# Kernel optimization log

Hardware: AMD Instinct MI355X
Metric: run time of the kernel (lower is better)

The kernel has to match this reference:

```python
import jax, jax.numpy as jnp
import numpy as np

B, S, H, OUT, L = 32, 4096, 128, 128, 3


def _log_g(x):
    return jnp.where(x >= 0, jnp.log(jax.nn.relu(x) + 0.5), -jax.nn.softplus(-x))


def _cell(x, Wz, bz, Wh, bh):
    # x: [B, S, Din] -> h: [B, S, H]
    k = x @ Wz.T + bz                              # [B,S,H]
    log_z = -jax.nn.softplus(-k)
    log_coeffs = -jax.nn.softplus(k)
    # h_0 = zeros -> log_g(0) = log(0.5)
    log_h0 = jnp.full((x.shape[0], 1, k.shape[-1]), np.log(0.5), dtype=k.dtype)
    log_tilde_h = _log_g(x @ Wh.T + bh)
    log_values = jnp.concatenate([log_h0, log_z + log_tilde_h], axis=1)  # [B,S+1,H]
    # FAITHFUL to source: cumsum over the FEATURE axis (dim=-1), pad along seq
    a_star = jnp.pad(jnp.cumsum(log_coeffs, axis=-1), ((0, 0), (1, 0), (0, 0)))
    log_h = a_star + jax.lax.cumlogsumexp(log_values - a_star, axis=1)
    # torch forward applies sigmoid to the cell output, then drops the h_0 row
    return jax.nn.sigmoid(jnp.exp(log_h))[:, 1:, :]


def setup_inputs() -> dict:
    key = jax.random.key(0)
    ks = jax.random.split(key, 2 * L + 2)
    inp = {"x": jax.random.normal(ks[0], (B, S), dtype=jnp.float32)}
    for l in range(L):
        din = 1 if l == 0 else H
        inp[f"Wz{l}"] = jax.random.normal(ks[1 + 2 * l], (H, din), dtype=jnp.float32) * 0.02
        inp[f"bz{l}"] = jnp.zeros((H,), dtype=jnp.float32)
        inp[f"Wh{l}"] = jax.random.normal(ks[2 + 2 * l], (H, din), dtype=jnp.float32) * 0.02
        inp[f"bh{l}"] = jnp.zeros((H,), dtype=jnp.float32)
    inp["Wout"] = jax.random.normal(ks[-1], (OUT, H * S), dtype=jnp.float32) * (1.0 / np.sqrt(H * S))
    inp["bout"] = jnp.zeros((OUT,), dtype=jnp.float32)
    return inp


def reference(x, Wz0, bz0, Wh0, bh0, Wz1, bz1, Wh1, bh1, Wz2, bz2, Wh2, bh2, Wout, bout):
    h = x[:, :, None]  # [B,S,1]
    for (Wz, bz, Wh, bh) in ((Wz0, bz0, Wh0, bh0), (Wz1, bz1, Wh1, bh1), (Wz2, bz2, Wh2, bh2)):
        h = _cell(h, Wz, bz, Wh, bh)
    flat = h.reshape(h.shape[0], -1)  # [B, S*H]
    return flat @ Wout.T + bout       # [B, OUT]
```

## Files before the change

### kernel.cpp

```cpp
#include <hip/hip_runtime.h>
#include <hip/hip_bf16.h>
#include <math.h>

#define B_   32
#define S_   4096
#define H_   128
#define OUT_ 128
#define P_   (B_*S_)
#define NC_  64
#define CH_  (S_/NC_)
#define NKS_ 512
#define KTOT_ (H_*S_)
#define NEGINF_ (-__builtin_inff())
#define HTP_ 136

typedef __bf16 bf16x8 __attribute__((ext_vector_type(8)));
typedef float  f32x4  __attribute__((ext_vector_type(4)));
typedef unsigned short ushort8_t __attribute__((ext_vector_type(8)));

__device__ __forceinline__ float sp_(float x) {
  return __logf(1.f + __expf(x));
}
__device__ __forceinline__ float logg_(float x) {
  float t = (x >= 0.f) ? (x + 0.5f) : __builtin_amdgcn_rcpf(1.f + __expf(-x));
  return __logf(t);
}
__device__ __forceinline__ float lae_(float a, float b) {
  float m = fmaxf(a, b);
  float d = -fabsf(a - b);
  return m + __logf(1.f + __expf(d));
}
__device__ __forceinline__ float sigm_(float e) {
  return __builtin_amdgcn_rcpf(1.f + __expf(-e));
}
__device__ __forceinline__ unsigned short f2bf_(float f) {
  unsigned int u = __float_as_uint(f);
  u += 0x7fffu + ((u >> 16) & 1u);
  return (unsigned short)(u >> 16);
}

#define DPPADD_(v, ctrl, rmask) \
  ((v) + __int_as_float(__builtin_amdgcn_update_dpp( \
      0, __float_as_int(v), (ctrl), (rmask), 0xf, true)))
__device__ __forceinline__ float wscan_(float v) {
  v = DPPADD_(v, 0x111, 0xf);
  v = DPPADD_(v, 0x112, 0xf);
  v = DPPADD_(v, 0x114, 0xf);
  v = DPPADD_(v, 0x118, 0xf);
  v = DPPADD_(v, 0x142, 0xa);
  v = DPPADD_(v, 0x143, 0xc);
  return v;
}

__global__ __launch_bounds__(256) void convw2_kernel(
    const float* __restrict__ Wz1, const float* __restrict__ Wh1,
    const float* __restrict__ Wz2, const float* __restrict__ Wh2,
    unsigned short* __restrict__ Wc1, unsigned short* __restrict__ Wc2)
{
  int idx = blockIdx.x * 256 + threadIdx.x;
  Wc1[idx] = f2bf_(idx < 16384 ? Wz1[idx] : Wh1[idx - 16384]);
  Wc2[idx] = f2bf_(idx < 16384 ? Wz2[idx] : Wh2[idx - 16384]);
}

__global__ __launch_bounds__(256) void prep0t_kernel(
    const float* __restrict__ x,
    const float* __restrict__ Wz, const float* __restrict__ bz,
    const float* __restrict__ Wh, const float* __restrict__ bh,
    float* __restrict__ u, float* __restrict__ A, float* __restrict__ tot)
{
  __shared__ float tpart[4][128];
  int lane = threadIdx.x & 63, w = threadIdx.x >> 6;
  float wz0 = Wz[lane], wz1 = Wz[lane + 64];
  float bz0 = bz[lane], bz1 = bz[lane + 64];
  float wh0 = Wh[lane], wh1 = Wh[lane + 64];
  float bh0 = bh[lane], bh1 = bh[lane + 64];
  int blk = blockIdx.x;
  size_t base = (size_t)blk * (CH_ * H_);
  int pos0 = blk * CH_;
  float t0 = NEGINF_, t1 = NEGINF_;
  for (int j = 0; j < 16; ++j) {
    int i = j * 4 + w;
    float xv = x[pos0 + i];
    float k0 = fmaf(xv, wz0, bz0), k1 = fmaf(xv, wz1, bz1);
    float g0 = fmaf(xv, wh0, bh0), g1 = fmaf(xv, wh1, bh1);
    float lc0 = -sp_(k0), lc1 = -sp_(k1);
    float lv0 = k0 + lc0 + logg_(g0);
    float lv1 = k1 + lc1 + logg_(g1);
    float s0 = wscan_(lc0);
    float c0 = __shfl(s0, 63, 64);
    float s1 = wscan_(lc1) + c0;
    float u0 = lv0 - s0, u1 = lv1 - s1;
    size_t o = base + (size_t)i * H_;
    u[o + lane]      = u0;  u[o + 64 + lane] = u1;
    A[o + lane]      = s0;  A[o + 64 + lane] = s1;
    t0 = lae_(t0, u0); t1 = lae_(t1, u1);
  }
  tpart[w][lane] = t0; tpart[w][64 + lane] = t1;
  __syncthreads();
  if (w == 0) {
    int ch = lane;
    tot[(size_t)blk * H_ + ch] =
        lae_(lae_(tpart[0][ch], tpart[1][ch]), lae_(tpart[2][ch], tpart[3][ch]));
    ch = lane + 64;
    tot[(size_t)blk * H_ + ch] =
        lae_(lae_(tpart[0][ch], tpart[1][ch]), lae_(tpart[2][ch], tpart[3][ch]));
  }
}

__global__ __launch_bounds__(128) void scan2_kernel(
    const float* __restrict__ tot, float* __restrict__ carry)
{
  int b = blockIdx.x, ch = threadIdx.x;
  float r = -0.6931471805599453f;
  for (int c = 0; c < NC_; ++c) {
    size_t idx = (size_t)(b * NC_ + c) * H_ + ch;
    carry[idx] = r;
    r = lae_(r, tot[idx]);
  }
}

__global__ __launch_bounds__(256) void kb_kernel(
    const float* __restrict__ carry,
    const unsigned short* __restrict__ Wc,
    const float* __restrict__ bz, const float* __restrict__ bh,
    float* __restrict__ u, float* __restrict__ A,
    float* __restrict__ tot)
{
  __shared__ unsigned short hT[64][HTP_];
  __shared__ float kg[16][260];
  __shared__ float scr[32][128];
  __shared__ float thand[128];
  __shared__ float tpart[4][128];
  int tid = threadIdx.x;
  int lane = tid & 63, w = tid >> 6;
  int l15 = lane & 15, quad = lane >> 4;
  int half = tid >> 7, ch = tid & 127;
  int blk = blockIdx.x;
  size_t base = (size_t)blk * (CH_ * H_);

  if (half == 0) {
    float r = carry[(size_t)blk * H_ + ch];
    const float* up = u + base + ch;
    const float* Ap = A + base + ch;
    for (int i0 = 0; i0 < 32; i0 += 16) {
      float uv[16], av[16];
      #pragma unroll
      for (int i = 0; i < 16; ++i) { uv[i] = up[(i0 + i) * H_]; av[i] = Ap[(i0 + i) * H_]; }
      #pragma unroll
      for (int i = 0; i < 16; ++i) {
        r = lae_(r, uv[i]);
        hT[i0 + i][ch] = f2bf_(sigm_(__expf(av[i] + r)));
      }
    }
    thand[ch] = r;
  } else {
    float r = NEGINF_;
    const float* up = u + base + ch;
    for (int i0 = 0; i0 < 32; i0 += 16) {
      float uv[16];
      #pragma unroll
      for (int i = 0; i < 16; ++i) uv[i] = up[(32 + i0 + i) * H_];
      #pragma unroll
      for (int i = 0; i < 16; ++i) { r = lae_(r, uv[i]); scr[i0 + i][ch] = r; }
    }
  }
  __syncthreads();
  if (half == 1) {
    float r31 = thand[ch];
    const float* Ap = A + base + ch;
    for (int i0 = 0; i0 < 32; i0 += 16) {
      float av[16];
      #pragma unroll
      for (int i = 0; i < 16; ++i) av[i] = Ap[(32 + i0 + i) * H_];
      #pragma unroll
      for (int i = 0; i < 16; ++i) {
        float ri = lae_(r31, scr[i0 + i][ch]);
        hT[32 + i0 + i][ch] = f2bf_(sigm_(__expf(av[i] + ri)));
      }
    }
  }
  __syncthreads();

  float bz0v = bz[lane], bz1v = bz[lane + 64];
  float bh0v = bh[lane], bh1v = bh[lane + 64];
  float t0 = NEGINF_, t1 = NEGINF_;

  for (int t = 0; t < 4; ++t) {
    f32x4 z = {0.f, 0.f, 0.f, 0.f};
    f32x4 acc[4] = {z, z, z, z};
    #pragma unroll
    for (int kk = 0; kk < 4; ++kk) {
      bf16x8 a = *reinterpret_cast<const bf16x8*>(&hT[t * 16 + l15][kk * 32 + quad * 8]);
      #pragma unroll
      for (int nt = 0; nt < 4; ++nt) {
        int n = w * 64 + nt * 16 + l15;
        bf16x8 bf = *reinterpret_cast<const bf16x8*>(Wc + n * 128 + kk * 32 + quad * 8);
        acc[nt] = __builtin_amdgcn_mfma_f32_16x16x32_bf16(a, bf, acc[nt], 0, 0, 0);
      }
    }
    __syncthreads();
    #pragma unroll
    for (int nt = 0; nt < 4; ++nt) {
      int col = w * 64 + nt * 16 + l15;
      #pragma unroll
      for (int r2 = 0; r2 < 4; ++r2)
        kg[quad * 4 + r2][col] = acc[nt][r2];
    }
    __syncthreads();
    #pragma unroll
    for (int i = 0; i < 4; ++i) {
      int row = w + i * 4;
      int sIdx = t * 16 + row;
      float k0 = kg[row][lane]        + bz0v;
      float k1 = kg[row][64 + lane]   + bz1v;
      float g0 = kg[row][128 + lane]  + bh0v;
      float g1 = kg[row][192 + lane]  + bh1v;
      float lc0 = -sp_(k0), lc1 = -sp_(k1);
      float lv0 = k0 + lc0 + logg_(g0);
      float lv1 = k1 + lc1 + logg_(g1);
      float s0 = wscan_(lc0);
      float c0 = __shfl(s0, 63, 64);
      float s1 = wscan_(lc1) + c0;
      float u0 = lv0 - s0, u1 = lv1 - s1;
      size_t o = base + (size_t)sIdx * H_;
      u[o + lane]      = u0;  u[o + 64 + lane] = u1;
      A[o + lane]      = s0;  A[o + 64 + lane] = s1;
      t0 = lae_(t0, u0); t1 = lae_(t1, u1);
    }
  }

  tpart[w][lane] = t0; tpart[w][64 + lane] = t1;
  __syncthreads();
  if (w == 0) {
    int c = lane;
    tot[(size_t)blk * H_ + c] =
        lae_(lae_(tpart[0][c], tpart[1][c]), lae_(tpart[2][c], tpart[3][c]));
    c = lane + 64;
    tot[(size_t)blk * H_ + c] =
        lae_(lae_(tpart[0][c], tpart[1][c]), lae_(tpart[2][c], tpart[3][c]));
  }
}

__global__ __launch_bounds__(256) void scan3v2_kernel(
    const float* __restrict__ u, const float* __restrict__ A,
    const float* __restrict__ carry, unsigned short* __restrict__ hbf)
{
  __shared__ float scr[32][128];
  __shared__ float thand[128];
  int tid = threadIdx.x;
  int half = tid >> 7, ch = tid & 127;
  int blk = blockIdx.x;
  size_t base = (size_t)blk * (CH_ * H_);
  const float* up = u + base + ch;
  const float* Ap = A + base + ch;
  unsigned short* hp = hbf + base + ch;
  if (half == 0) {
    float r = carry[(size_t)blk * H_ + ch];
    for (int i0 = 0; i0 < 32; i0 += 16) {
      float uv[16], av[16];
      #pragma unroll
      for (int i = 0; i < 16; ++i) { uv[i] = up[(i0 + i) * H_]; av[i] = Ap[(i0 + i) * H_]; }
      #pragma unroll
      for (int i = 0; i < 16; ++i) {
        r = lae_(r, uv[i]);
        hp[(size_t)(i0 + i) * H_] = f2bf_(sigm_(__expf(av[i] + r)));
      }
    }
    thand[ch] = r;
  } else {
    float r = NEGINF_;
    for (int i0 = 0; i0 < 32; i0 += 16) {
      float uv[16];
      #pragma unroll
      for (int i = 0; i < 16; ++i) uv[i] = up[(32 + i0 + i) * H_];
      #pragma unroll
      for (int i = 0; i < 16; ++i) { r = lae_(r, uv[i]); scr[i0 + i][ch] = r; }
    }
  }
  __syncthreads();
  if (half == 1) {
    float r31 = thand[ch];
    for (int i0 = 0; i0 < 32; i0 += 16) {
      float av[16];
      #pragma unroll
      for (int i = 0; i < 16; ++i) av[i] = Ap[(32 + i0 + i) * H_];
      #pragma unroll
      for (int i = 0; i < 16; ++i) {
        float ri = lae_(r31, scr[i0 + i][ch]);
        hp[(size_t)(32 + i0 + i) * H_] = f2bf_(sigm_(__expf(av[i] + ri)));
      }
    }
  }
}

__global__ __launch_bounds__(256) void outmm_kernel(
    const unsigned short* __restrict__ hbf,
    const float* __restrict__ Wout,
    float* __restrict__ part)
{
  const int KSL = KTOT_ / NKS_;
  int tid = threadIdx.x, w = tid >> 6, lane = tid & 63;
  int l15 = lane & 15, quad = lane >> 4;
  int k0base = blockIdx.x * KSL;
  f32x4 acc[2][2] = {{{0,0,0,0},{0,0,0,0}},{{0,0,0,0},{0,0,0,0}}};
  for (int ks = 0; ks < KSL; ks += 32) {
    int k0 = k0base + ks;
    bf16x8 a0 = *reinterpret_cast<const bf16x8*>(
        hbf + (size_t)l15 * KTOT_ + k0 + quad * 8);
    bf16x8 a1 = *reinterpret_cast<const bf16x8*>(
        hbf + (size_t)(16 + l15) * KTOT_ + k0 + quad * 8);
    #pragma unroll
    for (int nt = 0; nt < 2; ++nt) {
      int n = w * 32 + nt * 16 + l15;
      const float* wp = Wout + (size_t)n * KTOT_ + k0 + quad * 8;
      float4 wa = *reinterpret_cast<const float4*>(wp);
      float4 wb = *reinterpret_cast<const float4*>(wp + 4);
      ushort8_t tt;
      tt[0] = f2bf_(wa.x); tt[1] = f2bf_(wa.y); tt[2] = f2bf_(wa.z); tt[3] = f2bf_(wa.w);
      tt[4] = f2bf_(wb.x); tt[5] = f2bf_(wb.y); tt[6] = f2bf_(wb.z); tt[7] = f2bf_(wb.w);
      bf16x8 bf = __builtin_bit_cast(bf16x8, tt);
      acc[0][nt] = __builtin_amdgcn_mfma_f32_16x16x32_bf16(a0, bf, acc[0][nt], 0, 0, 0);
      acc[1][nt] = __builtin_amdgcn_mfma_f32_16x16x32_bf16(a1, bf, acc[1][nt], 0, 0, 0);
    }
  }
  float* pp = part + (size_t)blockIdx.x * (B_ * OUT_);
  #pragma unroll
  for (int mt = 0; mt < 2; ++mt)
    #pragma unroll
    for (int nt = 0; nt < 2; ++nt)
      #pragma unroll
      for (int r = 0; r < 4; ++r) {
        int b = mt * 16 + quad * 4 + r;
        int o = w * 32 + nt * 16 + l15;
        pp[b * OUT_ + o] = acc[mt][nt][r];
      }
}

__global__ __launch_bounds__(256) void outred_kernel(
    const float* __restrict__ part, const float* __restrict__ bout,
    float* __restrict__ out)
{
  int w = threadIdx.x >> 6, lane = threadIdx.x & 63;
  int idx = blockIdx.x * 4 + w;
  float s = 0.f;
  for (int wg = lane; wg < NKS_; wg += 64) s += part[(size_t)wg * (B_ * OUT_) + idx];
  #pragma unroll
  for (int d = 32; d; d >>= 1) s += __shfl_down(s, (unsigned)d, 64);
  if (lane == 0) out[idx] = s + bout[idx & (OUT_ - 1)];
}

extern "C" void kernel_launch(void* const* d_in, const int* in_sizes, int n_in,
                              void* d_out, int out_size, void* d_ws, size_t ws_size,
                              hipStream_t stream)
{
  const float* x    = (const float*)d_in[0];
  const float* Wz[3] = {(const float*)d_in[1], (const float*)d_in[5], (const float*)d_in[9]};
  const float* bz[3] = {(const float*)d_in[2], (const float*)d_in[6], (const float*)d_in[10]};
  const float* Wh[3] = {(const float*)d_in[3], (const float*)d_in[7], (const float*)d_in[11]};
  const float* bh[3] = {(const float*)d_in[4], (const float*)d_in[8], (const float*)d_in[12]};
  const float* Wout = (const float*)d_in[13];
  const float* bout = (const float*)d_in[14];
  float* out = (float*)d_out;

  char* ws = (char*)d_ws;
  float*          u     = (float*)(ws + 0);
  float*          A     = (float*)(ws + 67108864);
  unsigned short* hbf   = (unsigned short*)(ws + 134217728);
  unsigned short* Wc1   = (unsigned short*)(ws + 167772160);
  unsigned short* Wc2   = (unsigned short*)(ws + 167837696);
  float*          tot   = (float*)(ws + 167903232);
  float*          carry = (float*)(ws + 168951808);
  float*          part  = (float*)(ws + 170000384);

  convw2_kernel<<<128, 256, 0, stream>>>(Wz[1], Wh[1], Wz[2], Wh[2], Wc1, Wc2);

  prep0t_kernel<<<B_ * NC_, 256, 0, stream>>>(x, Wz[0], bz[0], Wh[0], bh[0], u, A, tot);
  scan2_kernel<<<B_, 128, 0, stream>>>(tot, carry);

  kb_kernel<<<B_ * NC_, 256, 0, stream>>>(carry, Wc1, bz[1], bh[1], u, A, tot);
  scan2_kernel<<<B_, 128, 0, stream>>>(tot, carry);
  kb_kernel<<<B_ * NC_, 256, 0, stream>>>(carry, Wc2, bz[2], bh[2], u, A, tot);
  scan2_kernel<<<B_, 128, 0, stream>>>(tot, carry);

  scan3v2_kernel<<<B_ * NC_, 256, 0, stream>>>(u, A, carry, hbf);

  outmm_kernel<<<NKS_, 256, 0, stream>>>(hbf, Wout, part);
  outred_kernel<<<(B_ * OUT_) / 4, 256, 0, stream>>>(part, bout, out);
}
```

Baseline: 670.1 us.

## Fold chunk-carry scans into consumer kernels and merge weight conversion into prep

Drops the three serial scan2 launches: each kb and scan3 block now computes its own carry by log-sum-exp reducing the chunk totals of all preceding chunks in its batch, using ping-pong total buffers. The weight bf16 conversion is folded into the layer-0 prep kernel as extra blocks, and the kg/scr shared arrays are unioned to cut LDS use. This removes launches and a low-parallelism serial pass (32 blocks doing 64 dependent steps) at the cost of redundant prefix reductions (up to 63 loads per channel per block).

```diff
diff --git a/kernel.cpp b/kernel.cpp
--- a/kernel.cpp
+++ b/kernel.cpp
@@ -13,6 +13,7 @@
 #define KTOT_ (H_*S_)
 #define NEGINF_ (-__builtin_inff())
 #define HTP_ 136
+#define LOGHALF_ (-0.6931471805599453f)
 
 typedef __bf16 bf16x8 __attribute__((ext_vector_type(8)));
 typedef float  f32x4  __attribute__((ext_vector_type(4)));
@@ -52,23 +53,22 @@
   return v;
 }
 
-__global__ __launch_bounds__(256) void convw2_kernel(
+__global__ __launch_bounds__(256) void prep0c_kernel(
+    const float* __restrict__ x,
+    const float* __restrict__ Wz, const float* __restrict__ bz,
+    const float* __restrict__ Wh, const float* __restrict__ bh,
+    float* __restrict__ u, float* __restrict__ A, float* __restrict__ tot,
     const float* __restrict__ Wz1, const float* __restrict__ Wh1,
     const float* __restrict__ Wz2, const float* __restrict__ Wh2,
     unsigned short* __restrict__ Wc1, unsigned short* __restrict__ Wc2)
 {
-  int idx = blockIdx.x * 256 + threadIdx.x;
-  Wc1[idx] = f2bf_(idx < 16384 ? Wz1[idx] : Wh1[idx - 16384]);
-  Wc2[idx] = f2bf_(idx < 16384 ? Wz2[idx] : Wh2[idx - 16384]);
-}
-
-__global__ __launch_bounds__(256) void prep0t_kernel(
-    const float* __restrict__ x,
-    const float* __restrict__ Wz, const float* __restrict__ bz,
-    const float* __restrict__ Wh, const float* __restrict__ bh,
-    float* __restrict__ u, float* __restrict__ A, float* __restrict__ tot)
-{
   __shared__ float tpart[4][128];
+  if (blockIdx.x >= 2048) {
+    int idx = (blockIdx.x - 2048) * 256 + threadIdx.x;
+    Wc1[idx] = f2bf_(idx < 16384 ? Wz1[idx] : Wh1[idx - 16384]);
+    Wc2[idx] = f2bf_(idx < 16384 ? Wz2[idx] : Wh2[idx - 16384]);
+    return;
+  }
   int lane = threadIdx.x & 63, w = threadIdx.x >> 6;
   float wz0 = Wz[lane], wz1 = Wz[lane + 64];
   float bz0 = bz[lane], bz1 = bz[lane + 64];
@@ -107,28 +107,18 @@
   }
 }
 
-__global__ __launch_bounds__(128) void scan2_kernel(
-    const float* __restrict__ tot, float* __restrict__ carry)
-{
-  int b = blockIdx.x, ch = threadIdx.x;
-  float r = -0.6931471805599453f;
-  for (int c = 0; c < NC_; ++c) {
-    size_t idx = (size_t)(b * NC_ + c) * H_ + ch;
-    carry[idx] = r;
-    r = lae_(r, tot[idx]);
-  }
-}
-
 __global__ __launch_bounds__(256) void kb_kernel(
-    const float* __restrict__ carry,
+    const float* __restrict__ totIn,
     const unsigned short* __restrict__ Wc,
     const float* __restrict__ bz, const float* __restrict__ bh,
     float* __restrict__ u, float* __restrict__ A,
-    float* __restrict__ tot)
+    float* __restrict__ totOut)
 {
   __shared__ unsigned short hT[64][HTP_];
-  __shared__ float kg[16][260];
-  __shared__ float scr[32][128];
+  __shared__ union {
+    float kg[16][260];
+    float scr[32][128];
+  } ks;
   __shared__ float thand[128];
   __shared__ float tpart[4][128];
   int tid = threadIdx.x;
@@ -136,10 +126,27 @@
   int l15 = lane & 15, quad = lane >> 4;
   int half = tid >> 7, ch = tid & 127;
   int blk = blockIdx.x;
+  int cidx = blk & (NC_ - 1);
   size_t base = (size_t)blk * (CH_ * H_);
 
+  {
+    const float* tp = totIn + (size_t)(blk - cidx) * H_ + ch;
+    float p0 = NEGINF_, p1 = NEGINF_;
+    int i = half;
+    for (; i + 2 < cidx; i += 4) {
+      float a0 = tp[(size_t)i * H_];
+      float a1 = tp[(size_t)(i + 2) * H_];
+      p0 = lae_(p0, a0); p1 = lae_(p1, a1);
+    }
+    for (; i < cidx; i += 2) p0 = lae_(p0, tp[(size_t)i * H_]);
+    tpart[half * 2][ch] = p0; tpart[half * 2 + 1][ch] = p1;
+  }
+  __syncthreads();
+
   if (half == 0) {
-    float r = carry[(size_t)blk * H_ + ch];
+    float r = LOGHALF_;
+    r = lae_(r, tpart[0][ch]); r = lae_(r, tpart[1][ch]);
+    r = lae_(r, tpart[2][ch]); r = lae_(r, tpart[3][ch]);
     const float* up = u + base + ch;
     const float* Ap = A + base + ch;
     for (int i0 = 0; i0 < 32; i0 += 16) {
@@ -161,7 +168,7 @@
       #pragma unroll
       for (int i = 0; i < 16; ++i) uv[i] = up[(32 + i0 + i) * H_];
       #pragma unroll
-      for (int i = 0; i < 16; ++i) { r = lae_(r, uv[i]); scr[i0 + i][ch] = r; }
+      for (int i = 0; i < 16; ++i) { r = lae_(r, uv[i]); ks.scr[i0 + i][ch] = r; }
     }
   }
   __syncthreads();
@@ -174,7 +181,7 @@
       for (int i = 0; i < 16; ++i) av[i] = Ap[(32 + i0 + i) * H_];
       #pragma unroll
       for (int i = 0; i < 16; ++i) {
-        float ri = lae_(r31, scr[i0 + i][ch]);
+        float ri = lae_(r31, ks.scr[i0 + i][ch]);
         hT[32 + i0 + i][ch] = f2bf_(sigm_(__expf(av[i] + ri)));
       }
     }
@@ -204,17 +211,17 @@
       int col = w * 64 + nt * 16 + l15;
       #pragma unroll
       for (int r2 = 0; r2 < 4; ++r2)
-        kg[quad * 4 + r2][col] = acc[nt][r2];
+        ks.kg[quad * 4 + r2][col] = acc[nt][r2];
     }
     __syncthreads();
     #pragma unroll
     for (int i = 0; i < 4; ++i) {
       int row = w + i * 4;
       int sIdx = t * 16 + row;
-      float k0 = kg[row][lane]        + bz0v;
-      float k1 = kg[row][64 + lane]   + bz1v;
-      float g0 = kg[row][128 + lane]  + bh0v;
-      float g1 = kg[row][192 + lane]  + bh1v;
+      float k0 = ks.kg[row][lane]        + bz0v;
+      float k1 = ks.kg[row][64 + lane]   + bz1v;
+      float g0 = ks.kg[row][128 + lane]  + bh0v;
+      float g1 = ks.kg[row][192 + lane]  + bh1v;
       float lc0 = -sp_(k0), lc1 = -sp_(k1);
       float lv0 = k0 + lc0 + logg_(g0);
       float lv1 = k1 + lc1 + logg_(g1);
@@ -233,29 +240,48 @@
   __syncthreads();
   if (w == 0) {
     int c = lane;
-    tot[(size_t)blk * H_ + c] =
+    totOut[(size_t)blk * H_ + c] =
         lae_(lae_(tpart[0][c], tpart[1][c]), lae_(tpart[2][c], tpart[3][c]));
     c = lane + 64;
-    tot[(size_t)blk * H_ + c] =
+    totOut[(size_t)blk * H_ + c] =
         lae_(lae_(tpart[0][c], tpart[1][c]), lae_(tpart[2][c], tpart[3][c]));
   }
 }
 
 __global__ __launch_bounds__(256) void scan3v2_kernel(
     const float* __restrict__ u, const float* __restrict__ A,
-    const float* __restrict__ carry, unsigned short* __restrict__ hbf)
+    const float* __restrict__ totIn, unsigned short* __restrict__ hbf)
 {
   __shared__ float scr[32][128];
   __shared__ float thand[128];
+  __shared__ float tpart[4][128];
   int tid = threadIdx.x;
   int half = tid >> 7, ch = tid & 127;
   int blk = blockIdx.x;
+  int cidx = blk & (NC_ - 1);
   size_t base = (size_t)blk * (CH_ * H_);
   const float* up = u + base + ch;
   const float* Ap = A + base + ch;
   unsigned short* hp = hbf + base + ch;
+
+  {
+    const float* tp = totIn + (size_t)(blk - cidx) * H_ + ch;
+    float p0 = NEGINF_, p1 = NEGINF_;
+    int i = half;
+    for (; i + 2 < cidx; i += 4) {
+      float a0 = tp[(size_t)i * H_];
+      float a1 = tp[(size_t)(i + 2) * H_];
+      p0 = lae_(p0, a0); p1 = lae_(p1, a1);
+    }
+    for (; i < cidx; i += 2) p0 = lae_(p0, tp[(size_t)i * H_]);
+    tpart[half * 2][ch] = p0; tpart[half * 2 + 1][ch] = p1;
+  }
+  __syncthreads();
+
   if (half == 0) {
-    float r = carry[(size_t)blk * H_ + ch];
+    float r = LOGHALF_;
+    r = lae_(r, tpart[0][ch]); r = lae_(r, tpart[1][ch]);
+    r = lae_(r, tpart[2][ch]); r = lae_(r, tpart[3][ch]);
     for (int i0 = 0; i0 < 32; i0 += 16) {
       float uv[16], av[16];
       #pragma unroll
@@ -368,21 +394,18 @@
   unsigned short* hbf   = (unsigned short*)(ws + 134217728);
   unsigned short* Wc1   = (unsigned short*)(ws + 167772160);
   unsigned short* Wc2   = (unsigned short*)(ws + 167837696);
-  float*          tot   = (float*)(ws + 167903232);
-  float*          carry = (float*)(ws + 168951808);
+  float*          totA  = (float*)(ws + 167903232);
+  float*          totB  = (float*)(ws + 168951808);
   float*          part  = (float*)(ws + 170000384);
 
-  convw2_kernel<<<128, 256, 0, stream>>>(Wz[1], Wh[1], Wz[2], Wh[2], Wc1, Wc2);
-
-  prep0t_kernel<<<B_ * NC_, 256, 0, stream>>>(x, Wz[0], bz[0], Wh[0], bh[0], u, A, tot);
-  scan2_kernel<<<B_, 128, 0, stream>>>(tot, carry);
-
-  kb_kernel<<<B_ * NC_, 256, 0, stream>>>(carry, Wc1, bz[1], bh[1], u, A, tot);
-  scan2_kernel<<<B_, 128, 0, stream>>>(tot, carry);
-  kb_kernel<<<B_ * NC_, 256, 0, stream>>>(carry, Wc2, bz[2], bh[2], u, A, tot);
-  scan2_kernel<<<B_, 128, 0, stream>>>(tot, carry);
-
-  scan3v2_kernel<<<B_ * NC_, 256, 0, stream>>>(u, A, carry, hbf);
+  prep0c_kernel<<<B_ * NC_ + 128, 256, 0, stream>>>(
+      x, Wz[0], bz[0], Wh[0], bh[0], u, A, totA,
+      Wz[1], Wh[1], Wz[2], Wh[2], Wc1, Wc2);
+
+  kb_kernel<<<B_ * NC_, 256, 0, stream>>>(totA, Wc1, bz[1], bh[1], u, A, totB);
+  kb_kernel<<<B_ * NC_, 256, 0, stream>>>(totB, Wc2, bz[2], bh[2], u, A, totA);
+
+  scan3v2_kernel<<<B_ * NC_, 256, 0, stream>>>(u, A, totA, hbf);
 
   outmm_kernel<<<NKS_, 256, 0, stream>>>(hbf, Wout, part);
   outred_kernel<<<(B_ * OUT_) / 4, 256, 0, stream>>>(part, bout, out);
```

New measurement: 658.6 us. About the same (-1.7%).
